# Kernel tuning notes

Measured on AMD Instinct MI355X. Metric: run time of the kernel, lower is better.

The kernel has to match this reference:

```python
import jax, jax.numpy as jnp
import numpy as np

N_HEADS = 16
D_QK = 64
D_MODEL = 1024
LN_EPS = 1e-6
B, QL, KVL = 2, 2048, 2048


def rms_norm(x, weight, eps=LN_EPS):
    var = jnp.mean(jnp.square(x.astype(jnp.float32)), axis=-1, keepdims=True)
    return (x * jax.lax.rsqrt(var + eps)).astype(x.dtype) * weight


def setup_inputs() -> dict:
    key = jax.random.key(0)
    ks = jax.random.split(key, 5)
    scale_h = 1.0 / np.sqrt(D_MODEL)
    return {
        "q_hidden_states": jax.random.normal(ks[0], (B, QL, D_MODEL), jnp.float32),
        "q_sequence_mask": jnp.ones((B, QL), dtype=bool),
        "kv_hidden_states": jax.random.normal(ks[1], (B, KVL, D_MODEL), jnp.float32),
        "kv_sequence_mask": jnp.ones((B, KVL), dtype=bool),
        "w_q": jax.random.normal(ks[2], (D_MODEL, N_HEADS * D_QK), jnp.float32) * scale_h,
        "w_kv": jax.random.normal(ks[3], (D_MODEL, 2 * N_HEADS * D_QK), jnp.float32) * scale_h,
        "w_o": jax.random.normal(ks[4], (N_HEADS * D_QK, D_MODEL), jnp.float32) * scale_h,
        "ln_weight": jnp.ones((D_MODEL,), jnp.float32),
    }


def reference(q_hidden_states, q_sequence_mask, kv_hidden_states, kv_sequence_mask,
              w_q, w_kv, w_o, ln_weight):
    b, ql, _ = q_hidden_states.shape
    kvl = kv_hidden_states.shape[1]

    normed = rms_norm(q_hidden_states, ln_weight)

    # q projection: [b, ql, H*D] -> [b, H, ql, D]
    q = (normed @ w_q).reshape(b, ql, N_HEADS, D_QK).transpose(0, 2, 1, 3)
    # kv projection: [b, kvl, 2*H*D] -> k, v each [b, H, kvl, D]
    kv = (kv_hidden_states @ w_kv).reshape(b, kvl, 2, N_HEADS, D_QK)
    k = kv[:, :, 0].transpose(0, 2, 1, 3)
    v = kv[:, :, 1].transpose(0, 2, 1, 3)

    # T5 attention: no 1/sqrt(d) scaling
    scores = jnp.einsum("bhqd,bhkd->bhqk", q, k)  # [b, H, ql, kvl]
    attn_mask = q_sequence_mask[:, None, :, None] & kv_sequence_mask[:, None, None, :]
    scores = jnp.where(attn_mask, scores, jnp.finfo(jnp.float32).min)
    attn = jax.nn.softmax(scores.astype(jnp.float32), axis=-1).astype(q.dtype)

    out = jnp.einsum("bhqk,bhkd->bhqd", attn, v)  # [b, H, ql, D]
    out = out.transpose(0, 2, 1, 3).reshape(b, ql, N_HEADS * D_QK)
    out = out @ w_o
    return q_hidden_states + out
```

## Files before the change

### kernel.cpp

```cpp
#include <hip/hip_runtime.h>
#include <stdint.h>

#define BSZ 2
#define QL 2048
#define KVL 2048
#define NH 16
#define DQK 64
#define DM 1024

typedef __bf16 bf16x8 __attribute__((ext_vector_type(8)));
typedef float f32x4 __attribute__((ext_vector_type(4)));

__device__ __forceinline__ ushort f2bf(float f) {
    union { float f; uint32_t u; } c; c.f = f;
    uint32_t u = c.u;
    return (ushort)((u + 0x7fffu + ((u >> 16) & 1u)) >> 16);
}

__device__ __forceinline__ uint32_t pack2bf(float lo, float hi) {
    union { float f; uint32_t u; } a, b;
    a.f = lo; b.f = hi;
    return __builtin_amdgcn_perm(b.u + 0x8000u, a.u + 0x8000u, 0x07060302u);
}

#define GLOAD_LDS16(g, l)                                              \
    __builtin_amdgcn_global_load_lds(                                  \
        (const __attribute__((address_space(1))) uint32_t*)(g),        \
        (__attribute__((address_space(3))) uint32_t*)(l), 16, 0, 0)

__global__ __launch_bounds__(256) void rmsnorm_cast_k(const float* __restrict__ x,
                                                      const float* __restrict__ w,
                                                      ushort* __restrict__ out) {
    int row = blockIdx.x;
    const float4* xr = (const float4*)(x + (size_t)row * DM);
    float4 v = xr[threadIdx.x];
    float s = v.x * v.x + v.y * v.y + v.z * v.z + v.w * v.w;
#pragma unroll
    for (int off = 32; off > 0; off >>= 1) s += __shfl_down(s, off, 64);
    __shared__ float ws4[4];
    if ((threadIdx.x & 63) == 0) ws4[threadIdx.x >> 6] = s;
    __syncthreads();
    float tot = ws4[0] + ws4[1] + ws4[2] + ws4[3];
    float r = rsqrtf(tot * (1.0f / DM) + 1e-6f);
    float4 wv = ((const float4*)w)[threadIdx.x];
    ushort4 o;
    o.x = f2bf(v.x * r * wv.x);
    o.y = f2bf(v.y * r * wv.y);
    o.z = f2bf(v.z * r * wv.z);
    o.w = f2bf(v.w * r * wv.w);
    ((ushort4*)(out + (size_t)row * DM))[threadIdx.x] = o;
}

__global__ __launch_bounds__(256) void prep_k(const float* __restrict__ kv_in,
                                              ushort* __restrict__ kvb,
                                              const float* __restrict__ w_q,
                                              const float* __restrict__ w_kv,
                                              const float* __restrict__ w_o,
                                              ushort* __restrict__ wqT,
                                              ushort* __restrict__ wkvT,
                                              ushort* __restrict__ woT) {
    __shared__ ushort tile[64][65];
    int blk = blockIdx.x;
    int tid = threadIdx.x;
    if (blk < 4096) {
        int i = blk * 256 + tid;
        float4 v = ((const float4*)kv_in)[i];
        ushort4 r;
        r.x = f2bf(v.x); r.y = f2bf(v.y); r.z = f2bf(v.z); r.w = f2bf(v.w);
        ((ushort4*)kvb)[i] = r;
        return;
    }
    int bi = blk - 4096;
    const float* in; ushort* out; int N, bx, by;
    const int K = 1024;
    if (bi < 256)      { in = w_q;  out = wqT;  N = 1024; bx = bi & 15; by = bi >> 4; }
    else if (bi < 768) { int j = bi - 256; in = w_kv; out = wkvT; N = 2048; bx = j & 31; by = j >> 5; }
    else               { int j = bi - 768; in = w_o;  out = woT;  N = 1024; bx = j & 15; by = j >> 4; }
    int k0 = by * 64, n0 = bx * 64;
    int colBase = tid & 63;
    int rowOff = tid >> 6;
#pragma unroll
    for (int i = 0; i < 16; ++i) {
        int row = i * 4 + rowOff;
        tile[colBase][row] = f2bf(in[(size_t)(k0 + row) * N + n0 + colBase]);
    }
    __syncthreads();
#pragma unroll
    for (int i = 0; i < 16; ++i) {
        int nrow = i * 4 + rowOff;
        out[(size_t)(n0 + nrow) * K + k0 + colBase] = tile[nrow][colBase];
    }
}

__global__ __launch_bounds__(256) void transpose_v_k(const ushort* __restrict__ v,
                                                     ushort* __restrict__ vt) {
    int bh = blockIdx.y;
    int t0 = blockIdx.x * 64;
    int lane = threadIdx.x & 63, wave = threadIdx.x >> 6;
    const ushort* src = v + (size_t)bh * KVL * DQK;
    ushort* dst = vt + (size_t)bh * DQK * KVL;
    int t = t0 + lane;
    int tp = (t & ~28) | ((t & 16) >> 2) | ((t & 4) << 1) | ((t & 8) << 1);
#pragma unroll
    for (int it = 0; it < 2; ++it) {
        int d0 = (wave * 2 + it) * 8;
        union { uint4 u; ushort s[8]; } val;
        val.u = *(const uint4*)&src[(size_t)t * DQK + d0];
#pragma unroll
        for (int j = 0; j < 8; ++j)
            dst[(size_t)(d0 + j) * KVL + tp] = val.s[j];
    }
}

__global__ __launch_bounds__(256) void gemm_qkv_k(
    const ushort* __restrict__ normed, const ushort* __restrict__ kvb,
    const ushort* __restrict__ wqT, const ushort* __restrict__ wkvT,
    ushort* __restrict__ q_out, ushort* __restrict__ k_out, ushort* __restrict__ v_out) {
    __shared__ __align__(16) ushort As[128 * 32];
    __shared__ __align__(16) ushort Bs[128 * 32];
    const int K = DM;
    int tid = threadIdx.x;
    int wave = tid >> 6, lane = tid & 63, quad = lane >> 4, l16 = lane & 15;
    int bx = blockIdx.x;
    int isQ = bx < 8;
    const ushort* A = isQ ? normed : kvb;
    const ushort* Bt = isQ ? wqT : wkvT;
    int n0 = (isQ ? bx : bx - 8) * 128;
    int m0 = blockIdx.y * 128;
    int wm = (wave & 1) * 64, wn = (wave >> 1) * 64;

    int r0 = tid >> 2, c0 = (tid & 3) << 3;
    const ushort* ga0 = &A[(size_t)(m0 + r0) * K + c0];
    const ushort* gb0 = &Bt[(size_t)(n0 + r0) * K + c0];

    f32x4 zero = {0.f, 0.f, 0.f, 0.f};
    f32x4 acc[4][4];
#pragma unroll
    for (int i = 0; i < 4; ++i)
#pragma unroll
        for (int j = 0; j < 4; ++j) acc[i][j] = zero;

    for (int k0 = 0; k0 < K; k0 += 32) {
        GLOAD_LDS16(ga0 + k0, &As[tid * 8]);
        GLOAD_LDS16(ga0 + (size_t)64 * K + k0, &As[(tid + 256) * 8]);
        GLOAD_LDS16(gb0 + k0, &Bs[tid * 8]);
        GLOAD_LDS16(gb0 + (size_t)64 * K + k0, &Bs[(tid + 256) * 8]);
        __syncthreads();
        bf16x8 af[4], bfr[4];
#pragma unroll
        for (int mi = 0; mi < 4; ++mi)
            af[mi] = *(const bf16x8*)(&As[(wm + mi * 16 + l16) * 32 + quad * 8]);
#pragma unroll
        for (int ni = 0; ni < 4; ++ni)
            bfr[ni] = *(const bf16x8*)(&Bs[(wn + ni * 16 + l16) * 32 + quad * 8]);
#pragma unroll
        for (int mi = 0; mi < 4; ++mi)
#pragma unroll
            for (int ni = 0; ni < 4; ++ni)
                acc[mi][ni] = __builtin_amdgcn_mfma_f32_16x16x32_bf16(
                    af[mi], bfr[ni], acc[mi][ni], 0, 0, 0);
        __syncthreads();
    }

    const float L2E = 1.44269504089f;
#pragma unroll
    for (int mi = 0; mi < 4; ++mi) {
#pragma unroll
        for (int ni = 0; ni < 4; ++ni) {
#pragma unroll
            for (int r = 0; r < 4; ++r) {
                int mm = m0 + wm + mi * 16 + quad * 4 + r;
                int nn = n0 + wn + ni * 16 + l16;
                float val = acc[mi][ni][r];
                int b = mm >> 11, t = mm & 2047;
                if (isQ) {
                    int h = nn >> 6, d = nn & 63;
                    q_out[((size_t)((b << 4) | h) * QL + t) * DQK + d] = f2bf(val * L2E);
                } else {
                    int c = nn >> 10, h = (nn >> 6) & 15, d = nn & 63;
                    ushort* dst = c ? v_out : k_out;
                    dst[((size_t)((b << 4) | h) * KVL + t) * DQK + d] = f2bf(val);
                }
            }
        }
    }
}

__global__ __launch_bounds__(256) void gemm_o_k(const ushort* __restrict__ A,
                                                const ushort* __restrict__ Bt,
                                                const float* __restrict__ resid,
                                                float* __restrict__ f_out) {
    __shared__ __align__(16) ushort As[64 * 32];
    __shared__ __align__(16) ushort Bs[128 * 32];
    const int K = DM;
    int tid = threadIdx.x;
    int wave = tid >> 6, lane = tid & 63, quad = lane >> 4, l16 = lane & 15;
    int n0 = blockIdx.x * 128, m0 = blockIdx.y * 64;
    int wm = (wave & 1) * 32, wn = (wave >> 1) * 64;

    int r0 = tid >> 2, c0 = (tid & 3) << 3;
    const ushort* ga0 = &A[(size_t)(m0 + r0) * K + c0];
    const ushort* gb0 = &Bt[(size_t)(n0 + r0) * K + c0];

    f32x4 zero = {0.f, 0.f, 0.f, 0.f};
    f32x4 acc[2][4];
#pragma unroll
    for (int i = 0; i < 2; ++i)
#pragma unroll
        for (int j = 0; j < 4; ++j) acc[i][j] = zero;

    for (int k0 = 0; k0 < K; k0 += 32) {
        GLOAD_LDS16(ga0 + k0, &As[tid * 8]);
        GLOAD_LDS16(gb0 + k0, &Bs[tid * 8]);
        GLOAD_LDS16(gb0 + (size_t)64 * K + k0, &Bs[(tid + 256) * 8]);
        __syncthreads();
        bf16x8 af[2], bfr[4];
#pragma unroll
        for (int mi = 0; mi < 2; ++mi)
            af[mi] = *(const bf16x8*)(&As[(wm + mi * 16 + l16) * 32 + quad * 8]);
#pragma unroll
        for (int ni = 0; ni < 4; ++ni)
            bfr[ni] = *(const bf16x8*)(&Bs[(wn + ni * 16 + l16) * 32 + quad * 8]);
#pragma unroll
        for (int mi = 0; mi < 2; ++mi)
#pragma unroll
            for (int ni = 0; ni < 4; ++ni)
                acc[mi][ni] = __builtin_amdgcn_mfma_f32_16x16x32_bf16(
                    af[mi], bfr[ni], acc[mi][ni], 0, 0, 0);
        __syncthreads();
    }

#pragma unroll
    for (int mi = 0; mi < 2; ++mi) {
#pragma unroll
        for (int ni = 0; ni < 4; ++ni) {
#pragma unroll
            for (int r = 0; r < 4; ++r) {
                int mm = m0 + wm + mi * 16 + quad * 4 + r;
                int nn = n0 + wn + ni * 16 + l16;
                size_t o = (size_t)mm * DM + nn;
                f_out[o] = resid[o] + acc[mi][ni][r];
            }
        }
    }
}

__global__ __launch_bounds__(256) void attn_k(const ushort* __restrict__ qh,
                                              const ushort* __restrict__ kh,
                                              const ushort* __restrict__ vt,
                                              ushort* __restrict__ ao) {
    __shared__ __align__(16) ushort smem[128 * 72];
    char* KsB = (char*)smem;
    char* VsB = (char*)smem + 8192;
    int bh = blockIdx.y, bI = bh >> 4, hI = bh & 15;
    int q0 = blockIdx.x * 128;
    int tid = threadIdx.x, wave = tid >> 6, lane = tid & 63;
    int quad = lane >> 4, l16 = lane & 15;
    const ushort* Qp = qh + (size_t)bh * QL * DQK;
    const ushort* Kp = kh + (size_t)bh * KVL * DQK;
    const ushort* Vp = vt + (size_t)bh * DQK * KVL;

    bf16x8 qf[2][2];
#pragma unroll
    for (int g = 0; g < 2; ++g) {
        const ushort* qrow = Qp + (size_t)(q0 + wave * 32 + g * 16 + l16) * DQK;
        qf[g][0] = *(const bf16x8*)(qrow + quad * 8);
        qf[g][1] = *(const bf16x8*)(qrow + 32 + quad * 8);
    }

    int srow = tid >> 3;
    int scol = (tid & 7) << 3;
    int stoff = srow * 128 + (((tid & 7) << 4) ^ ((srow & 7) << 4));
    int xr7 = (l16 & 7) << 4;
    int ko0 = (quad * 16) ^ xr7;
    int ko1 = (quad * 16 + 64) ^ xr7;

    f32x4 zero = {0.f, 0.f, 0.f, 0.f};
    f32x4 o[2][4];
#pragma unroll
    for (int g = 0; g < 2; ++g)
#pragma unroll
        for (int i = 0; i < 4; ++i) o[g][i] = zero;
    float lsum[2] = {0.f, 0.f};

    uint4 kr0 = *(const uint4*)&Kp[(size_t)srow * DQK + scol];
    uint4 kr1 = *(const uint4*)&Kp[(size_t)(srow + 32) * DQK + scol];
    uint4 vr0 = *(const uint4*)&Vp[(size_t)srow * KVL + scol];
    uint4 vr1 = *(const uint4*)&Vp[(size_t)(srow + 32) * KVL + scol];

    for (int t0 = 0; t0 < KVL; t0 += 64) {
        *(uint4*)(KsB + stoff) = kr0;
        *(uint4*)(KsB + 4096 + stoff) = kr1;
        *(uint4*)(VsB + stoff) = vr0;
        *(uint4*)(VsB + 4096 + stoff) = vr1;
        __syncthreads();
        int tn = t0 + 64;
        if (tn < KVL) {
            kr0 = *(const uint4*)&Kp[(size_t)(tn + srow) * DQK + scol];
            kr1 = *(const uint4*)&Kp[(size_t)(tn + srow + 32) * DQK + scol];
            vr0 = *(const uint4*)&Vp[(size_t)srow * KVL + tn + scol];
            vr1 = *(const uint4*)&Vp[(size_t)(srow + 32) * KVL + tn + scol];
        }

        f32x4 s[2][4];
#pragma unroll
        for (int mi = 0; mi < 4; ++mi) {
            const char* kb = KsB + (mi * 16 + l16) * 128;
            bf16x8 kf0 = *(const bf16x8*)(kb + ko0);
            bf16x8 kf1 = *(const bf16x8*)(kb + ko1);
#pragma unroll
            for (int g = 0; g < 2; ++g) {
                f32x4 a = zero;
                a = __builtin_amdgcn_mfma_f32_16x16x32_bf16(kf0, qf[g][0], a, 0, 0, 0);
                a = __builtin_amdgcn_mfma_f32_16x16x32_bf16(kf1, qf[g][1], a, 0, 0, 0);
                s[g][mi] = a;
            }
        }

        bf16x8 pf[2][2];
#pragma unroll
        for (int g = 0; g < 2; ++g) {
            float rs = 0.f;
            uint32_t pw[8];
#pragma unroll
            for (int mi = 0; mi < 4; ++mi) {
                float e0 = __builtin_amdgcn_exp2f(s[g][mi][0]);
                float e1 = __builtin_amdgcn_exp2f(s[g][mi][1]);
                float e2 = __builtin_amdgcn_exp2f(s[g][mi][2]);
                float e3 = __builtin_amdgcn_exp2f(s[g][mi][3]);
                rs += (e0 + e1) + (e2 + e3);
                asm("v_cvt_pk_bf16_f32 %0, %1, %2" : "=v"(pw[mi * 2]) : "v"(e0), "v"(e1));
                asm("v_cvt_pk_bf16_f32 %0, %1, %2" : "=v"(pw[mi * 2 + 1]) : "v"(e2), "v"(e3));
            }
            lsum[g] += rs;
            union { uint32_t u[4]; bf16x8 v; } b0, b1;
            b0.u[0] = pw[0]; b0.u[1] = pw[1]; b0.u[2] = pw[2]; b0.u[3] = pw[3];
            b1.u[0] = pw[4]; b1.u[1] = pw[5]; b1.u[2] = pw[6]; b1.u[3] = pw[7];
            pf[g][0] = b0.v;
            pf[g][1] = b1.v;
        }

#pragma unroll
        for (int mi = 0; mi < 4; ++mi) {
            const char* vb = VsB + (mi * 16 + l16) * 128;
            bf16x8 vf0 = *(const bf16x8*)(vb + ko0);
            bf16x8 vf1 = *(const bf16x8*)(vb + ko1);
#pragma unroll
            for (int g = 0; g < 2; ++g) {
                o[g][mi] = __builtin_amdgcn_mfma_f32_16x16x32_bf16(vf0, pf[g][0], o[g][mi], 0, 0, 0);
                o[g][mi] = __builtin_amdgcn_mfma_f32_16x16x32_bf16(vf1, pf[g][1], o[g][mi], 0, 0, 0);
            }
        }
        __syncthreads();
    }

#pragma unroll
    for (int g = 0; g < 2; ++g) {
        float lg = lsum[g];
        lg += __shfl_xor(lg, 16, 64);
        lg += __shfl_xor(lg, 32, 64);
        float rinv = __builtin_amdgcn_rcpf(lg);
        ushort* orow = &smem[(size_t)(wave * 32 + g * 16 + l16) * 72];
#pragma unroll
        for (int mi = 0; mi < 4; ++mi) {
            uint2 pk;
            pk.x = pack2bf(o[g][mi][0] * rinv, o[g][mi][1] * rinv);
            pk.y = pack2bf(o[g][mi][2] * rinv, o[g][mi][3] * rinv);
            *(uint2*)&orow[mi * 16 + quad * 4] = pk;
        }
    }
    __syncthreads();
#pragma unroll
    for (int it = 0; it < 4; ++it) {
        int idx = tid + it * 256;
        int ql = idx >> 3, c = (idx & 7) << 3;
        uint4 vv = *(const uint4*)&smem[ql * 72 + c];
        *(uint4*)&ao[((size_t)(bI * QL + q0 + ql)) * DM + hI * 64 + c] = vv;
    }
}

extern "C" void kernel_launch(void* const* d_in, const int* in_sizes, int n_in,
                              void* d_out, int out_size, void* d_ws, size_t ws_size,
                              hipStream_t stream) {
    (void)in_sizes; (void)n_in; (void)out_size; (void)ws_size;
    const float* qh_in = (const float*)d_in[0];
    const float* kv_in = (const float*)d_in[2];
    const float* w_q  = (const float*)d_in[4];
    const float* w_kv = (const float*)d_in[5];
    const float* w_o  = (const float*)d_in[6];
    const float* lnw  = (const float*)d_in[7];
    float* out = (float*)d_out;

    char* ws = (char*)d_ws;
    ushort* normed = (ushort*)(ws);
    ushort* vT     = (ushort*)(ws);
    ushort* kvb    = (ushort*)(ws + ((size_t)8 << 20));
    ushort* wqT    = (ushort*)(ws + ((size_t)16 << 20));
    ushort* wkvT   = (ushort*)(ws + ((size_t)18 << 20));
    ushort* woT    = (ushort*)(ws + ((size_t)22 << 20));
    ushort* qheads = (ushort*)(ws + ((size_t)24 << 20));
    ushort* kheads = (ushort*)(ws + ((size_t)32 << 20));
    ushort* vheads = (ushort*)(ws + ((size_t)40 << 20));
    ushort* attno  = (ushort*)(ws + ((size_t)48 << 20));

    rmsnorm_cast_k<<<BSZ * QL, 256, 0, stream>>>(qh_in, lnw, normed);
    prep_k<<<4096 + 1024, 256, 0, stream>>>(kv_in, kvb, w_q, w_kv, w_o, wqT, wkvT, woT);

    gemm_qkv_k<<<dim3(24, 32), 256, 0, stream>>>(normed, kvb, wqT, wkvT,
                                                 qheads, kheads, vheads);
    transpose_v_k<<<dim3(KVL / 64, BSZ * NH), 256, 0, stream>>>(vheads, vT);
    attn_k<<<dim3(QL / 128, BSZ * NH), 256, 0, stream>>>(qheads, kheads, vT, attno);
    gemm_o_k<<<dim3(8, 64), 256, 0, stream>>>(attno, woT, qh_in, out);
}
```

Baseline: 209.2 us.

## Merge rmsnorm into prep kernel and double GEMM K-tile with XOR-swizzled LDS

Folds the rmsnorm cast into the weight/kv prep kernel so one launch does all input conversion, which removes a kernel launch. Both projection GEMMs now stage a 64-wide K slice per iteration instead of 32, halving the number of barriers. LDS columns are XOR-swizzled per row to avoid bank conflicts on the fragment reads. The cost is doubled LDS per block, which may lower occupancy.

```diff
diff --git a/kernel.cpp b/kernel.cpp
--- a/kernel.cpp
+++ b/kernel.cpp
@@ -28,49 +28,49 @@
         (const __attribute__((address_space(1))) uint32_t*)(g),        \
         (__attribute__((address_space(3))) uint32_t*)(l), 16, 0, 0)
 
-__global__ __launch_bounds__(256) void rmsnorm_cast_k(const float* __restrict__ x,
-                                                      const float* __restrict__ w,
-                                                      ushort* __restrict__ out) {
-    int row = blockIdx.x;
-    const float4* xr = (const float4*)(x + (size_t)row * DM);
-    float4 v = xr[threadIdx.x];
-    float s = v.x * v.x + v.y * v.y + v.z * v.z + v.w * v.w;
-#pragma unroll
-    for (int off = 32; off > 0; off >>= 1) s += __shfl_down(s, off, 64);
-    __shared__ float ws4[4];
-    if ((threadIdx.x & 63) == 0) ws4[threadIdx.x >> 6] = s;
-    __syncthreads();
-    float tot = ws4[0] + ws4[1] + ws4[2] + ws4[3];
-    float r = rsqrtf(tot * (1.0f / DM) + 1e-6f);
-    float4 wv = ((const float4*)w)[threadIdx.x];
-    ushort4 o;
-    o.x = f2bf(v.x * r * wv.x);
-    o.y = f2bf(v.y * r * wv.y);
-    o.z = f2bf(v.z * r * wv.z);
-    o.w = f2bf(v.w * r * wv.w);
-    ((ushort4*)(out + (size_t)row * DM))[threadIdx.x] = o;
-}
-
-__global__ __launch_bounds__(256) void prep_k(const float* __restrict__ kv_in,
-                                              ushort* __restrict__ kvb,
-                                              const float* __restrict__ w_q,
-                                              const float* __restrict__ w_kv,
-                                              const float* __restrict__ w_o,
-                                              ushort* __restrict__ wqT,
-                                              ushort* __restrict__ wkvT,
-                                              ushort* __restrict__ woT) {
-    __shared__ ushort tile[64][65];
+__global__ __launch_bounds__(256) void prep_all_k(const float* __restrict__ x,
+                                                  const float* __restrict__ w,
+                                                  ushort* __restrict__ normed,
+                                                  const float* __restrict__ kv_in,
+                                                  ushort* __restrict__ kvb,
+                                                  const float* __restrict__ w_q,
+                                                  const float* __restrict__ w_kv,
+                                                  const float* __restrict__ w_o,
+                                                  ushort* __restrict__ wqT,
+                                                  ushort* __restrict__ wkvT,
+                                                  ushort* __restrict__ woT) {
+    __shared__ __align__(16) ushort tile[64][65];
     int blk = blockIdx.x;
     int tid = threadIdx.x;
     if (blk < 4096) {
-        int i = blk * 256 + tid;
+        float* ws4 = (float*)tile;
+        const float4* xr = (const float4*)(x + (size_t)blk * DM);
+        float4 v = xr[tid];
+        float s = v.x * v.x + v.y * v.y + v.z * v.z + v.w * v.w;
+#pragma unroll
+        for (int off = 32; off > 0; off >>= 1) s += __shfl_down(s, off, 64);
+        if ((tid & 63) == 0) ws4[tid >> 6] = s;
+        __syncthreads();
+        float tot = ws4[0] + ws4[1] + ws4[2] + ws4[3];
+        float r = rsqrtf(tot * (1.0f / DM) + 1e-6f);
+        float4 wv = ((const float4*)w)[tid];
+        ushort4 o;
+        o.x = f2bf(v.x * r * wv.x);
+        o.y = f2bf(v.y * r * wv.y);
+        o.z = f2bf(v.z * r * wv.z);
+        o.w = f2bf(v.w * r * wv.w);
+        ((ushort4*)(normed + (size_t)blk * DM))[tid] = o;
+        return;
+    }
+    if (blk < 8192) {
+        int i = (blk - 4096) * 256 + tid;
         float4 v = ((const float4*)kv_in)[i];
         ushort4 r;
         r.x = f2bf(v.x); r.y = f2bf(v.y); r.z = f2bf(v.z); r.w = f2bf(v.w);
         ((ushort4*)kvb)[i] = r;
         return;
     }
-    int bi = blk - 4096;
+    int bi = blk - 8192;
     const float* in; ushort* out; int N, bx, by;
     const int K = 1024;
     if (bi < 256)      { in = w_q;  out = wqT;  N = 1024; bx = bi & 15; by = bi >> 4; }
@@ -116,8 +116,8 @@
     const ushort* __restrict__ normed, const ushort* __restrict__ kvb,
     const ushort* __restrict__ wqT, const ushort* __restrict__ wkvT,
     ushort* __restrict__ q_out, ushort* __restrict__ k_out, ushort* __restrict__ v_out) {
-    __shared__ __align__(16) ushort As[128 * 32];
-    __shared__ __align__(16) ushort Bs[128 * 32];
+    __shared__ __align__(16) ushort As[128 * 64];
+    __shared__ __align__(16) ushort Bs[128 * 64];
     const int K = DM;
     int tid = threadIdx.x;
     int wave = tid >> 6, lane = tid & 63, quad = lane >> 4, l16 = lane & 15;
@@ -129,9 +129,11 @@
     int m0 = blockIdx.y * 128;
     int wm = (wave & 1) * 64, wn = (wave >> 1) * 64;
 
-    int r0 = tid >> 2, c0 = (tid & 3) << 3;
-    const ushort* ga0 = &A[(size_t)(m0 + r0) * K + c0];
-    const ushort* gb0 = &Bt[(size_t)(n0 + r0) * K + c0];
+    int r0 = tid >> 3;
+    int c0s = (((tid & 7) ^ (r0 & 7)) << 3);
+    const ushort* ga0 = &A[(size_t)(m0 + r0) * K + c0s];
+    const ushort* gb0 = &Bt[(size_t)(n0 + r0) * K + c0s];
+    int xr7 = (l16 & 7) << 4;
 
     f32x4 zero = {0.f, 0.f, 0.f, 0.f};
     f32x4 acc[4][4];
@@ -140,25 +142,30 @@
 #pragma unroll
         for (int j = 0; j < 4; ++j) acc[i][j] = zero;
 
-    for (int k0 = 0; k0 < K; k0 += 32) {
-        GLOAD_LDS16(ga0 + k0, &As[tid * 8]);
-        GLOAD_LDS16(ga0 + (size_t)64 * K + k0, &As[(tid + 256) * 8]);
-        GLOAD_LDS16(gb0 + k0, &Bs[tid * 8]);
-        GLOAD_LDS16(gb0 + (size_t)64 * K + k0, &Bs[(tid + 256) * 8]);
-        __syncthreads();
-        bf16x8 af[4], bfr[4];
-#pragma unroll
-        for (int mi = 0; mi < 4; ++mi)
-            af[mi] = *(const bf16x8*)(&As[(wm + mi * 16 + l16) * 32 + quad * 8]);
-#pragma unroll
-        for (int ni = 0; ni < 4; ++ni)
-            bfr[ni] = *(const bf16x8*)(&Bs[(wn + ni * 16 + l16) * 32 + quad * 8]);
-#pragma unroll
-        for (int mi = 0; mi < 4; ++mi)
+    for (int k0 = 0; k0 < K; k0 += 64) {
+#pragma unroll
+        for (int p = 0; p < 4; ++p) {
+            GLOAD_LDS16(ga0 + (size_t)(p * 32) * K + k0, &As[(tid + p * 256) * 8]);
+            GLOAD_LDS16(gb0 + (size_t)(p * 32) * K + k0, &Bs[(tid + p * 256) * 8]);
+        }
+        __syncthreads();
+#pragma unroll
+        for (int c = 0; c < 2; ++c) {
+            int off = (c * 64 + quad * 16) ^ xr7;
+            bf16x8 af[4], bfr[4];
+#pragma unroll
+            for (int mi = 0; mi < 4; ++mi)
+                af[mi] = *(const bf16x8*)((const char*)As + (wm + mi * 16 + l16) * 128 + off);
 #pragma unroll
             for (int ni = 0; ni < 4; ++ni)
-                acc[mi][ni] = __builtin_amdgcn_mfma_f32_16x16x32_bf16(
-                    af[mi], bfr[ni], acc[mi][ni], 0, 0, 0);
+                bfr[ni] = *(const bf16x8*)((const char*)Bs + (wn + ni * 16 + l16) * 128 + off);
+#pragma unroll
+            for (int mi = 0; mi < 4; ++mi)
+#pragma unroll
+                for (int ni = 0; ni < 4; ++ni)
+                    acc[mi][ni] = __builtin_amdgcn_mfma_f32_16x16x32_bf16(
+                        af[mi], bfr[ni], acc[mi][ni], 0, 0, 0);
+        }
         __syncthreads();
     }
 
@@ -190,17 +197,19 @@
                                                 const ushort* __restrict__ Bt,
                                                 const float* __restrict__ resid,
                                                 float* __restrict__ f_out) {
-    __shared__ __align__(16) ushort As[64 * 32];
-    __shared__ __align__(16) ushort Bs[128 * 32];
+    __shared__ __align__(16) ushort As[64 * 64];
+    __shared__ __align__(16) ushort Bs[128 * 64];
     const int K = DM;
     int tid = threadIdx.x;
     int wave = tid >> 6, lane = tid & 63, quad = lane >> 4, l16 = lane & 15;
     int n0 = blockIdx.x * 128, m0 = blockIdx.y * 64;
     int wm = (wave & 1) * 32, wn = (wave >> 1) * 64;
 
-    int r0 = tid >> 2, c0 = (tid & 3) << 3;
-    const ushort* ga0 = &A[(size_t)(m0 + r0) * K + c0];
-    const ushort* gb0 = &Bt[(size_t)(n0 + r0) * K + c0];
+    int r0 = tid >> 3;
+    int c0s = (((tid & 7) ^ (r0 & 7)) << 3);
+    const ushort* ga0 = &A[(size_t)(m0 + r0) * K + c0s];
+    const ushort* gb0 = &Bt[(size_t)(n0 + r0) * K + c0s];
+    int xr7 = (l16 & 7) << 4;
 
     f32x4 zero = {0.f, 0.f, 0.f, 0.f};
     f32x4 acc[2][4];
@@ -209,24 +218,31 @@
 #pragma unroll
         for (int j = 0; j < 4; ++j) acc[i][j] = zero;
 
-    for (int k0 = 0; k0 < K; k0 += 32) {
-        GLOAD_LDS16(ga0 + k0, &As[tid * 8]);
-        GLOAD_LDS16(gb0 + k0, &Bs[tid * 8]);
-        GLOAD_LDS16(gb0 + (size_t)64 * K + k0, &Bs[(tid + 256) * 8]);
-        __syncthreads();
-        bf16x8 af[2], bfr[4];
-#pragma unroll
-        for (int mi = 0; mi < 2; ++mi)
-            af[mi] = *(const bf16x8*)(&As[(wm + mi * 16 + l16) * 32 + quad * 8]);
-#pragma unroll
-        for (int ni = 0; ni < 4; ++ni)
-            bfr[ni] = *(const bf16x8*)(&Bs[(wn + ni * 16 + l16) * 32 + quad * 8]);
-#pragma unroll
-        for (int mi = 0; mi < 2; ++mi)
+    for (int k0 = 0; k0 < K; k0 += 64) {
+#pragma unroll
+        for (int p = 0; p < 2; ++p)
+            GLOAD_LDS16(ga0 + (size_t)(p * 32) * K + k0, &As[(tid + p * 256) * 8]);
+#pragma unroll
+        for (int p = 0; p < 4; ++p)
+            GLOAD_LDS16(gb0 + (size_t)(p * 32) * K + k0, &Bs[(tid + p * 256) * 8]);
+        __syncthreads();
+#pragma unroll
+        for (int c = 0; c < 2; ++c) {
+            int off = (c * 64 + quad * 16) ^ xr7;
+            bf16x8 af[2], bfr[4];
+#pragma unroll
+            for (int mi = 0; mi < 2; ++mi)
+                af[mi] = *(const bf16x8*)((const char*)As + (wm + mi * 16 + l16) * 128 + off);
 #pragma unroll
             for (int ni = 0; ni < 4; ++ni)
-                acc[mi][ni] = __builtin_amdgcn_mfma_f32_16x16x32_bf16(
-                    af[mi], bfr[ni], acc[mi][ni], 0, 0, 0);
+                bfr[ni] = *(const bf16x8*)((const char*)Bs + (wn + ni * 16 + l16) * 128 + off);
+#pragma unroll
+            for (int mi = 0; mi < 2; ++mi)
+#pragma unroll
+                for (int ni = 0; ni < 4; ++ni)
+                    acc[mi][ni] = __builtin_amdgcn_mfma_f32_16x16x32_bf16(
+                        af[mi], bfr[ni], acc[mi][ni], 0, 0, 0);
+        }
         __syncthreads();
     }
 
@@ -403,9 +419,8 @@
     ushort* vheads = (ushort*)(ws + ((size_t)40 << 20));
     ushort* attno  = (ushort*)(ws + ((size_t)48 << 20));
 
-    rmsnorm_cast_k<<<BSZ * QL, 256, 0, stream>>>(qh_in, lnw, normed);
-    prep_k<<<4096 + 1024, 256, 0, stream>>>(kv_in, kvb, w_q, w_kv, w_o, wqT, wkvT, woT);
-
+    prep_all_k<<<4096 + 4096 + 1024, 256, 0, stream>>>(qh_in, lnw, normed, kv_in, kvb,
+                                                       w_q, w_kv, w_o, wqT, wkvT, woT);
     gemm_qkv_k<<<dim3(24, 32), 256, 0, stream>>>(normed, kvb, wqT, wkvT,
                                                  qheads, kheads, vheads);
     transpose_v_k<<<dim3(KVL / 64, BSZ * NH), 256, 0, stream>>>(vheads, vT);
```

New measurement: 207.8 us. About the same (-0.6%).
